# Kernel tuning notes

Hardware: AMD Instinct MI355X
Metric: run time of the kernel (lower is better)

## Reference

```python
import jax, jax.numpy as jnp
import numpy as np
from jax import lax

B = 2
H = W = 128          # resolution
N = H * W            # 16384 tokens
C = 128              # in_channels
C2 = C // 2          # 64, attention dim
G = 16               # window_size
HEADS = 8
HDIM = C2 // HEADS   # 8
EPS = 1e-5
DN = ('NCHW', 'OIHW', 'NCHW')


def setup_inputs():
    key = jax.random.key(0)
    ks = jax.random.split(key, 16)
    r = lambda i, shape, s=0.02: jax.random.normal(ks[i], shape, jnp.float32) * s
    z = lambda shape: jnp.zeros(shape, jnp.float32)
    o = lambda shape: jnp.ones(shape, jnp.float32)
    return {
        'x_C': jax.random.normal(ks[0], (B, N, C), jnp.float32),
        'x_T': jax.random.normal(ks[1], (B, N, C), jnp.float32),
        # S_conv = depthwise 3x3 + pointwise 1x1
        'conv1_dw': r(2, (C, 1, 3, 3)), 'conv1_dw_b': z((C,)),
        'conv1_pw': r(3, (C, C, 1, 1)), 'conv1_pw_b': z((C,)),
        'bn1_gamma': o((C,)), 'bn1_beta': z((C,)),
        'bn1_mean': r(4, (C,), 0.1), 'bn1_var': jnp.abs(r(5, (C,), 0.1)) + 1.0,
        'enc_W': r(6, (C, C2)), 'enc_b': z((C2,)),
        'pos': r(7, (1, N, C2)),
        'ln_gamma': o((C2,)), 'ln_beta': z((C2,)),
        'qkv_W': r(8, (C2, 3 * C2)),                      # qkv_bias=False
        'proj_W': r(9, (C2, C2)), 'proj_b': z((C2,)),
        'ffn_W1': r(10, (C2, C2)), 'ffn_b1': z((C2,)),
        'ffn_W2': r(11, (C2, C2)), 'ffn_b2': z((C2,)),
        'dec_W': r(12, (C2, C)), 'dec_b': z((C,)),
    }


def _ln(x, g, b):
    m = jnp.mean(x, -1, keepdims=True)
    v = jnp.var(x, -1, keepdims=True)
    return (x - m) * jax.lax.rsqrt(v + EPS) * g + b


def _win_part(x):  # (B,N,C2) -> (B*nW, G*G, C2)
    x = x.reshape(B, H // G, G, W // G, G, C2).transpose(0, 1, 3, 2, 4, 5)
    return x.reshape(-1, G * G, C2)


def _win_rev(x):  # (B*nW, G*G, C2) -> (B,N,C2)
    x = x.reshape(B, H // G, W // G, G, G, C2).transpose(0, 1, 3, 2, 4, 5)
    return x.reshape(B, N, C2)


def reference(x_C, x_T, conv1_dw, conv1_dw_b, conv1_pw, conv1_pw_b,
              bn1_gamma, bn1_beta, bn1_mean, bn1_var,
              enc_W, enc_b, pos, ln_gamma, ln_beta, qkv_W,
              proj_W, proj_b, ffn_W1, ffn_b1, ffn_W2, ffn_b2, dec_W, dec_b):
    cb = lambda a: a[None, :, None, None]
    # ---- CNN branch on x_C: S_conv -> BN(eval) -> ReLU, residual
    xC = x_C.reshape(B, H, W, C).transpose(0, 3, 1, 2)  # NCHW
    h = lax.conv_general_dilated(xC, conv1_dw, (1, 1), 'SAME',
                                 feature_group_count=C, dimension_numbers=DN) + cb(conv1_dw_b)
    h = lax.conv_general_dilated(h, conv1_pw, (1, 1), 'SAME',
                                 dimension_numbers=DN) + cb(conv1_pw_b)
    h = (h - cb(bn1_mean)) * cb(bn1_gamma * jax.lax.rsqrt(bn1_var + EPS)) + cb(bn1_beta)
    x1 = jax.nn.relu(h) + xC
    # ---- x_T branch: source overwrites conv/bn outputs -> x2 = relu(x_T) + x_T
    xT = x_T.reshape(B, H, W, C).transpose(0, 3, 1, 2)
    x2 = jax.nn.relu(xT) + xT
    # ---- flatten to tokens, encode + positional embedding
    x = x1.transpose(0, 2, 3, 1).reshape(B, N, C)
    y = x2.transpose(0, 2, 3, 1).reshape(B, N, C)
    x_poi = x @ enc_W + enc_b + pos
    y_poi = y @ enc_W + enc_b + pos
    # ---- window partition + LayerNorm
    wx = _ln(_win_part(x_poi), ln_gamma, ln_beta)
    wy = _ln(_win_part(y_poi), ln_gamma, ln_beta)
    # ---- dual-stream windowed attention (cross values)
    scale = HDIM ** -0.5
    def qkv(t):
        q, k, v = jnp.split(t @ qkv_W, 3, axis=-1)
        re = lambda a: a.reshape(-1, G * G, HEADS, HDIM).transpose(0, 2, 1, 3)
        return re(q), re(k), re(v)
    q, k, v = qkv(wx)
    q1, k1, v1 = qkv(wy)
    attn = jax.nn.softmax(jnp.einsum('bhid,bhjd->bhij', q * scale, k), axis=-1)
    attn1 = jax.nn.softmax(jnp.einsum('bhid,bhjd->bhij', q1 * scale, k1), axis=-1)
    ox = jnp.einsum('bhij,bhjd->bhid', attn, v1).transpose(0, 2, 1, 3).reshape(-1, G * G, C2)
    oy = jnp.einsum('bhij,bhjd->bhid', attn1, v).transpose(0, 2, 1, 3).reshape(-1, G * G, C2)
    ox = ox @ proj_W + proj_b + wx
    oy = oy @ proj_W + proj_b + wy
    # ---- window reverse + FFN (pre-LN, residual)
    x = _win_rev(ox)
    y = _win_rev(oy)
    ffn = lambda t: jax.nn.relu(_ln(t, ln_gamma, ln_beta) @ ffn_W1 + ffn_b1) @ ffn_W2 + ffn_b2
    x = x + ffn(x)
    y = y + ffn(y)
    # ---- decode back to C channels; to_3d(reshape) is identity on (B,N,C)
    return (x @ dec_W + dec_b) + (y @ dec_W + dec_b)
```

## Files before the change

### kernel.cpp

```cpp
#include <hip/hip_runtime.h>
#include <hip/hip_bf16.h>
#include <math.h>

#define EPSF 1e-5f
#define KSCL 0.51010090329771713f

#if __has_builtin(__builtin_amdgcn_exp2f)
#define EXP2(x) __builtin_amdgcn_exp2f(x)
#else
#define EXP2(x) exp2f(x)
#endif

typedef __attribute__((ext_vector_type(8))) short short8;
typedef __attribute__((ext_vector_type(16))) float f32x16;

__device__ __forceinline__ float bf2f(unsigned short u) {
    union { unsigned int i; float f; } x; x.i = ((unsigned int)u) << 16; return x.f;
}
__device__ __forceinline__ unsigned int f2bf(float f) {
    union { float f; unsigned int i; } u; u.f = f;
    unsigned int r = u.i + 0x7FFFu + ((u.i >> 16) & 1u);
    return r >> 16;
}
__device__ __forceinline__ unsigned cvtpk(float a, float b) {
    unsigned r;
    asm("v_cvt_pk_bf16_f32 %0, %1, %2" : "=v"(r) : "v"(a), "v"(b));
    return r;
}
__device__ __forceinline__ void bbuild(const unsigned pk[8], int lh,
                                       short8& B0, short8& B1) {
    unsigned xs[8];
    #pragma unroll
    for (int i = 0; i < 8; ++i) xs[i] = (unsigned)__shfl_xor((int)pk[i], 32);
    uint4 w0, w1;
    w0.x = lh ? xs[2] : pk[0]; w0.y = lh ? xs[3] : pk[1];
    w0.z = lh ? pk[2] : xs[0]; w0.w = lh ? pk[3] : xs[1];
    w1.x = lh ? xs[6] : pk[4]; w1.y = lh ? xs[7] : pk[5];
    w1.z = lh ? pk[6] : xs[4]; w1.w = lh ? pk[7] : xs[5];
    B0 = __builtin_bit_cast(short8, w0);
    B1 = __builtin_bit_cast(short8, w1);
}

__global__ __launch_bounds__(256) void k_dwconv(
    const float* __restrict__ xC, const float* __restrict__ dwW,
    const float* __restrict__ dwB, unsigned short* __restrict__ xdwb,
    const float* __restrict__ qkvW, const float* __restrict__ pw,
    const float* __restrict__ pwb, const float* __restrict__ gam,
    const float* __restrict__ bet, const float* __restrict__ mean,
    const float* __restrict__ var, const float* __restrict__ projW,
    const float* __restrict__ W1, const float* __restrict__ W2,
    const float* __restrict__ decW, const float* __restrict__ encW,
    unsigned short* __restrict__ qkvWT, unsigned short* __restrict__ weff,
    float* __restrict__ beff, unsigned short* __restrict__ projWTn,
    unsigned short* __restrict__ W1Tn, unsigned short* __restrict__ W2Tn,
    unsigned short* __restrict__ decTn, unsigned short* __restrict__ encWTn)
{
    int tid = threadIdx.x;
    int bid = blockIdx.x;
    if (bid >= 1024) {
        int pid = (bid - 1024) * 256 + tid;
        if (pid < 12288) {
            int o = pid >> 6, c = pid & 63;
            qkvWT[pid] = (unsigned short)f2bf(qkvW[c * 192 + o]);
        } else if (pid < 28672) {
            int i = pid - 12288;
            int co = i >> 7;
            float sc = gam[co] * rsqrtf(var[co] + EPSF);
            weff[i] = (unsigned short)f2bf(pw[i] * sc);
        } else if (pid < 32768) {
            int i = pid - 28672, m = i >> 6, c = i & 63;
            projWTn[i] = (unsigned short)f2bf(projW[c * 64 + m]);
        } else if (pid < 36864) {
            int i = pid - 32768, m = i >> 6, c = i & 63;
            W1Tn[i] = (unsigned short)f2bf(W1[c * 64 + m]);
        } else if (pid < 40960) {
            int i = pid - 36864, m = i >> 6, c = i & 63;
            W2Tn[i] = (unsigned short)f2bf(W2[c * 64 + m]);
        } else if (pid < 49152) {
            int i = pid - 40960, m = i >> 6, c = i & 63;
            decTn[i] = (unsigned short)f2bf(decW[c * 128 + m]);
        } else if (pid < 57344) {
            int i = pid - 49152, m = i >> 7, c = i & 127;
            encWTn[i] = (unsigned short)f2bf(encW[c * 64 + m]);
        } else if (pid < 57472) {
            int i = pid - 57344;
            float sc = gam[i] * rsqrtf(var[i] + EPSF);
            beff[i] = (pwb[i] - mean[i]) * sc + bet[i];
        }
        return;
    }
    __shared__ float s_w[128 * 9];
    __shared__ float s_bias[128];
    for (int i = tid; i < 128 * 9; i += 256) s_w[i] = dwW[i];
    if (tid < 128) s_bias[tid] = dwB[tid];
    __syncthreads();
    int idx = bid * 256 + tid;
    int c4 = (idx & 31) * 4;
    int pg = idx >> 5;
    int t0 = pg * 4;
    int b = t0 >> 14, n = t0 & 16383;
    int row = n >> 7, col0 = n & 127;
    float vb[3][6][4];
    #pragma unroll
    for (int ky = 0; ky < 3; ++ky) {
        int r = row + ky - 1;
        #pragma unroll
        for (int cx = 0; cx < 6; ++cx) {
            int cl = col0 + cx - 1;
            if ((unsigned)r < 128u && (unsigned)cl < 128u) {
                *(float4*)&vb[ky][cx][0] =
                    *(const float4*)&xC[((size_t)(b << 14) + (r << 7) + cl) * 128 + c4];
            } else {
                vb[ky][cx][0] = 0.f; vb[ky][cx][1] = 0.f; vb[ky][cx][2] = 0.f; vb[ky][cx][3] = 0.f;
            }
        }
    }
    float acc[4][4];
    #pragma unroll
    for (int p = 0; p < 4; ++p)
        #pragma unroll
        for (int j = 0; j < 4; ++j) acc[p][j] = s_bias[c4 + j];
    #pragma unroll
    for (int ky = 0; ky < 3; ++ky)
        #pragma unroll
        for (int kx = 0; kx < 3; ++kx)
            #pragma unroll
            for (int j = 0; j < 4; ++j) {
                float w = s_w[(c4 + j) * 9 + ky * 3 + kx];
                #pragma unroll
                for (int p = 0; p < 4; ++p)
                    acc[p][j] = fmaf(w, vb[ky][p + kx][j], acc[p][j]);
            }
    #pragma unroll
    for (int p = 0; p < 4; ++p) {
        uint2 o;
        o.x = f2bf(acc[p][0]) | (f2bf(acc[p][1]) << 16);
        o.y = f2bf(acc[p][2]) | (f2bf(acc[p][3]) << 16);
        *(uint2*)&xdwb[((size_t)t0 + p) * 128 + c4] = o;
    }
}

__global__ __launch_bounds__(256) void k_pw(
    const unsigned short* __restrict__ xdwb, const float* __restrict__ xC,
    const unsigned short* __restrict__ weff, const float* __restrict__ beff,
    unsigned short* __restrict__ x1b)
{
    int tid = threadIdx.x;
    int wv = tid >> 6, lane = tid & 63, l31 = lane & 31, lh = lane >> 5;
    int wr = wv >> 1, wc = wv & 1;
    int T0 = blockIdx.x * 64;
    int ta = T0 + wr * 32 + l31;
    short8 af[8];
    #pragma unroll
    for (int ks = 0; ks < 8; ++ks)
        af[ks] = *(const short8*)&xdwb[(size_t)ta * 128 + ks * 16 + lh * 8];
    #pragma unroll
    for (int nt = 0; nt < 2; ++nt) {
        int co = wc * 64 + nt * 32 + l31;
        f32x16 acc = {};
        #pragma unroll
        for (int ks = 0; ks < 8; ++ks) {
            short8 bfr = *(const short8*)&weff[(size_t)co * 128 + ks * 16 + lh * 8];
            acc = __builtin_amdgcn_mfma_f32_32x32x16_bf16(af[ks], bfr, acc, 0, 0, 0);
        }
        float be = beff[co];
        #pragma unroll
        for (int r = 0; r < 16; ++r) {
            int tt = T0 + wr * 32 + (r & 3) + 8 * (r >> 2) + 4 * lh;
            float v = fmaxf(acc[r] + be, 0.f) + xC[(size_t)tt * 128 + co];
            x1b[(size_t)tt * 128 + co] = (unsigned short)f2bf(v);
        }
    }
}

__global__ __launch_bounds__(256) void k_encqkv(
    const unsigned short* __restrict__ x1b, const float* __restrict__ xT,
    const unsigned short* __restrict__ encWTn, const float* __restrict__ encb,
    const float* __restrict__ pos, const float* __restrict__ lng,
    const float* __restrict__ lnb, const unsigned short* __restrict__ qkvWT,
    unsigned short* __restrict__ wxb, unsigned short* __restrict__ wyb,
    unsigned short* __restrict__ qk, unsigned short* __restrict__ vT)
{
    int tid = threadIdx.x;
    int wv = tid >> 6, l31 = tid & 31, lh = (tid >> 5) & 1;
    int s = blockIdx.y;
    int T0 = blockIdx.x * 128;
    int t = T0 + wv * 32 + l31;
    int n = t & 16383;
    short8 bf[8];
    if (s == 0) {
        #pragma unroll
        for (int ks = 0; ks < 8; ++ks)
            bf[ks] = *(const short8*)&x1b[(size_t)t * 128 + ks * 16 + lh * 8];
    } else {
        #pragma unroll
        for (int ks = 0; ks < 8; ++ks) {
            float4 f0 = *(const float4*)&xT[(size_t)t * 128 + ks * 16 + lh * 8];
            float4 f1 = *(const float4*)&xT[(size_t)t * 128 + ks * 16 + lh * 8 + 4];
            float r0 = f0.x > 0.f ? 2.f * f0.x : f0.x;
            float r1 = f0.y > 0.f ? 2.f * f0.y : f0.y;
            float r2 = f0.z > 0.f ? 2.f * f0.z : f0.z;
            float r3 = f0.w > 0.f ? 2.f * f0.w : f0.w;
            float r4 = f1.x > 0.f ? 2.f * f1.x : f1.x;
            float r5 = f1.y > 0.f ? 2.f * f1.y : f1.y;
            float r6 = f1.z > 0.f ? 2.f * f1.z : f1.z;
            float r7 = f1.w > 0.f ? 2.f * f1.w : f1.w;
            uint4 w;
            w.x = cvtpk(r0, r1); w.y = cvtpk(r2, r3);
            w.z = cvtpk(r4, r5); w.w = cvtpk(r6, r7);
            bf[ks] = __builtin_bit_cast(short8, w);
        }
    }
    f32x16 xm[2];
    #pragma unroll
    for (int ta = 0; ta < 2; ++ta) {
        f32x16 acc = {};
        #pragma unroll
        for (int ks = 0; ks < 8; ++ks) {
            short8 af = *(const short8*)&encWTn[(size_t)(ta * 32 + l31) * 128 + ks * 16 + lh * 8];
            acc = __builtin_amdgcn_mfma_f32_32x32x16_bf16(af, bf[ks], acc, 0, 0, 0);
        }
        #pragma unroll
        for (int g = 0; g < 4; ++g) {
            int c0 = ta * 32 + g * 8 + lh * 4;
            float4 eb = *(const float4*)&encb[c0];
            float4 pv = *(const float4*)&pos[(size_t)n * 64 + c0];
            acc[g * 4 + 0] += eb.x + pv.x;
            acc[g * 4 + 1] += eb.y + pv.y;
            acc[g * 4 + 2] += eb.z + pv.z;
            acc[g * 4 + 3] += eb.w + pv.w;
        }
        xm[ta] = acc;
    }
    float sm = 0.f, sq = 0.f;
    #pragma unroll
    for (int ta = 0; ta < 2; ++ta)
        #pragma unroll
        for (int r = 0; r < 16; ++r) { float v = xm[ta][r]; sm += v; sq += v * v; }
    sm += __shfl_xor(sm, 32); sq += __shfl_xor(sq, 32);
    float mu = sm * (1.f / 64.f);
    float rs = rsqrtf(fmaxf(sq * (1.f / 64.f) - mu * mu, 0.f) + EPSF);
    unsigned short* dstb = s ? wyb : wxb;
    unsigned pku[2][8];
    #pragma unroll
    for (int ta = 0; ta < 2; ++ta)
        #pragma unroll
        for (int g = 0; g < 4; ++g) {
            int c0 = ta * 32 + g * 8 + lh * 4;
            float4 gg = *(const float4*)&lng[c0];
            float4 bb = *(const float4*)&lnb[c0];
            float u0 = (xm[ta][g * 4 + 0] - mu) * rs * gg.x + bb.x;
            float u1 = (xm[ta][g * 4 + 1] - mu) * rs * gg.y + bb.y;
            float u2 = (xm[ta][g * 4 + 2] - mu) * rs * gg.z + bb.z;
            float u3 = (xm[ta][g * 4 + 3] - mu) * rs * gg.w + bb.w;
            pku[ta][g * 2]     = cvtpk(u0, u1);
            pku[ta][g * 2 + 1] = cvtpk(u2, u3);
            uint2 o; o.x = pku[ta][g * 2]; o.y = pku[ta][g * 2 + 1];
            *(uint2*)&dstb[(size_t)t * 64 + c0] = o;
        }
    short8 Bu[4];
    bbuild(pku[0], lh, Bu[0], Bu[1]);
    bbuild(pku[1], lh, Bu[2], Bu[3]);
    int b = T0 >> 14;
    int row = (T0 & 16383) >> 7;
    int cp = wv * 32 + l31;
    int wid = ((row >> 4) << 3) + (cp >> 4);
    int p = ((row & 15) << 4) + (cp & 15);
    size_t cb = (size_t)(s * 2 + b) * 512 + wid;
    #pragma unroll
    for (int nt = 0; nt < 6; ++nt) {
        f32x16 acc = {};
        #pragma unroll
        for (int ks = 0; ks < 4; ++ks) {
            short8 afr = *(const short8*)&qkvWT[(size_t)(nt * 32 + l31) * 64 + ks * 16 + lh * 8];
            acc = __builtin_amdgcn_mfma_f32_32x32x16_bf16(afr, Bu[ks], acc, 0, 0, 0);
        }
        if (nt < 4) {
            const float scl = nt < 2 ? 1.f : KSCL;
            const int sec = nt < 2 ? 0 : 1;
            #pragma unroll
            for (int g = 0; g < 4; ++g) {
                int head = (nt & 1) * 4 + g;
                unsigned short* rec = qk + (cb + head * 64) * 4096;
                float f0 = acc[4 * g + 0] * scl, f1 = acc[4 * g + 1] * scl;
                float f2 = acc[4 * g + 2] * scl, f3 = acc[4 * g + 3] * scl;
                unsigned u01 = cvtpk(f0, f1), u23 = cvtpk(f2, f3);
                int off = p * 16 + sec * 8 + 4 * lh;
                *(unsigned*)(rec + off) = u01;
                *(unsigned*)(rec + off + 2) = u23;
            }
        } else {
            #pragma unroll
            for (int g = 0; g < 4; ++g) {
                int head = (nt - 4) * 4 + g;
                unsigned short* vrec = vT + (cb + head * 64) * 2048;
                int d0 = 4 * lh;
                vrec[(d0 + 0) * 256 + p] = (unsigned short)f2bf(acc[4 * g + 0]);
                vrec[(d0 + 1) * 256 + p] = (unsigned short)f2bf(acc[4 * g + 1]);
                vrec[(d0 + 2) * 256 + p] = (unsigned short)f2bf(acc[4 * g + 2]);
                vrec[(d0 + 3) * 256 + p] = (unsigned short)f2bf(acc[4 * g + 3]);
            }
        }
    }
}

__global__ __launch_bounds__(256) void k_attn(
    const unsigned short* __restrict__ qk, const unsigned short* __restrict__ vT,
    unsigned short* __restrict__ obx, unsigned short* __restrict__ oby)
{
    int tid = threadIdx.x;
    int wave = tid >> 6, lane = tid & 63;
    int lh = lane >> 5, l31 = lane & 31;
    int bx = blockIdx.x;
    int s = bx >> 10;
    int r = bx & 1023;
    int head = (r >> 6) & 7, wid = r & 63, b = r >> 9;
    const unsigned short* qbase = qk + ((size_t)s * 1024 + r) * 4096;
    const unsigned short* vbase = vT + ((size_t)(s ^ 1) * 1024 + r) * 2048;

    short8 qf[2];
    #pragma unroll
    for (int qt = 0; qt < 2; ++qt) {
        uint4 v = {0u, 0u, 0u, 0u};
        if (lh == 0) v = *(const uint4*)(qbase + (size_t)(wave * 64 + qt * 32 + l31) * 16);
        qf[qt] = __builtin_bit_cast(short8, v);
    }
    f32x16 acc[2];
    #pragma unroll
    for (int qt = 0; qt < 2; ++qt) acc[qt] = (f32x16){};
    const unsigned ONES = 0x3F803F80u;

    for (int jt = 0; jt < 8; ++jt) {
        uint4 kv = {0u, 0u, 0u, 0u};
        if (lh == 0) kv = *(const uint4*)(qbase + (size_t)(jt * 32 + l31) * 16 + 8);
        short8 kf = __builtin_bit_cast(short8, kv);
        uint2 a0 = {ONES, ONES}, a1 = {ONES, ONES}, a2 = {ONES, ONES}, a3 = {ONES, ONES};
        if (l31 < 8) {
            const unsigned short* vp = vbase + l31 * 256 + jt * 32 + lh * 4;
            a0 = *(const uint2*)vp;
            a1 = *(const uint2*)(vp + 8);
            a2 = *(const uint2*)(vp + 16);
            a3 = *(const uint2*)(vp + 24);
        }
        uint4 vaw = {a0.x, a0.y, a1.x, a1.y};
        uint4 vbw = {a2.x, a2.y, a3.x, a3.y};
        short8 vf0 = __builtin_bit_cast(short8, vaw);
        short8 vf1 = __builtin_bit_cast(short8, vbw);
        #pragma unroll
        for (int qt = 0; qt < 2; ++qt) {
            f32x16 c = __builtin_amdgcn_mfma_f32_32x32x16_bf16(kf, qf[qt], (f32x16){}, 0, 0, 0);
            float p[16];
            #pragma unroll
            for (int i = 0; i < 16; ++i) p[i] = EXP2(c[i]);
            unsigned pk[8];
            #pragma unroll
            for (int i = 0; i < 8; ++i) pk[i] = cvtpk(p[2 * i], p[2 * i + 1]);
            uint4 bw0 = {pk[0], pk[1], pk[2], pk[3]};
            uint4 bw1 = {pk[4], pk[5], pk[6], pk[7]};
            short8 B0 = __builtin_bit_cast(short8, bw0);
            short8 B1 = __builtin_bit_cast(short8, bw1);
            acc[qt] = __builtin_amdgcn_mfma_f32_32x32x16_bf16(vf0, B0, acc[qt], 0, 0, 0);
            acc[qt] = __builtin_amdgcn_mfma_f32_32x32x16_bf16(vf1, B1, acc[qt], 0, 0, 0);
        }
    }
    unsigned short* dst = s ? oby : obx;
    #pragma unroll
    for (int qt = 0; qt < 2; ++qt) {
        float inv = 1.f / acc[qt][4];
        int p = wave * 64 + qt * 32 + l31;
        int orow = (wid >> 3) * 16 + (p >> 4);
        int ocol = (wid & 7) * 16 + (p & 15);
        size_t t = (size_t)b * 16384 + orow * 128 + ocol;
        uint2 o;
        o.x = cvtpk(acc[qt][0] * inv, acc[qt][1] * inv);
        o.y = cvtpk(acc[qt][2] * inv, acc[qt][3] * inv);
        *(uint2*)&dst[t * 64 + head * 8 + lh * 4] = o;
    }
}

__global__ __launch_bounds__(256) void k_fusedec(
    const unsigned short* __restrict__ obx, const unsigned short* __restrict__ oby,
    const unsigned short* __restrict__ wxb, const unsigned short* __restrict__ wyb,
    const unsigned short* __restrict__ projWTn, const float* __restrict__ projb,
    const unsigned short* __restrict__ W1Tn, const float* __restrict__ b1,
    const unsigned short* __restrict__ W2Tn, const float* __restrict__ b2,
    const unsigned short* __restrict__ decTn, const float* __restrict__ decb,
    const float* __restrict__ lng, const float* __restrict__ lnb,
    float* __restrict__ out)
{
    int tid = threadIdx.x;
    int wv = tid >> 6, l31 = tid & 31, lh = (tid >> 5) & 1;
    int t = blockIdx.x * 128 + wv * 32 + l31;
    f32x16 zacc[2];
    zacc[0] = (f32x16){}; zacc[1] = (f32x16){};
    #pragma unroll 1
    for (int s = 0; s < 2; ++s) {
        const unsigned short* osrc = s ? oby : obx;
        const unsigned short* wsrc = s ? wyb : wxb;
        short8 bo[4];
        #pragma unroll
        for (int kap = 0; kap < 4; ++kap)
            bo[kap] = *(const short8*)&osrc[(size_t)t * 64 + kap * 16 + lh * 8];
        f32x16 a1[2];
        #pragma unroll
        for (int ta = 0; ta < 2; ++ta) {
            f32x16 acc = {};
            #pragma unroll
            for (int kap = 0; kap < 4; ++kap) {
                short8 af = *(const short8*)&projWTn[(size_t)(ta * 32 + l31) * 64 + kap * 16 + lh * 8];
                acc = __builtin_amdgcn_mfma_f32_32x32x16_bf16(af, bo[kap], acc, 0, 0, 0);
            }
            #pragma unroll
            for (int g = 0; g < 4; ++g) {
                int c0 = ta * 32 + g * 8 + lh * 4;
                float4 pb = *(const float4*)&projb[c0];
                uint2 wr2 = *(const uint2*)&wsrc[(size_t)t * 64 + c0];
                acc[g * 4 + 0] += pb.x + bf2f((unsigned short)(wr2.x & 0xffffu));
                acc[g * 4 + 1] += pb.y + bf2f((unsigned short)(wr2.x >> 16));
                acc[g * 4 + 2] += pb.z + bf2f((unsigned short)(wr2.y & 0xffffu));
                acc[g * 4 + 3] += pb.w + bf2f((unsigned short)(wr2.y >> 16));
            }
            a1[ta] = acc;
        }
        float sm = 0.f, sq = 0.f;
        #pragma unroll
        for (int ta = 0; ta < 2; ++ta)
            #pragma unroll
            for (int r = 0; r < 16; ++r) { float v = a1[ta][r]; sm += v; sq += v * v; }
        sm += __shfl_xor(sm, 32); sq += __shfl_xor(sq, 32);
        float mu = sm * (1.f / 64.f);
        float rs = rsqrtf(fmaxf(sq * (1.f / 64.f) - mu * mu, 0.f) + EPSF);
        unsigned pku[2][8];
        #pragma unroll
        for (int ta = 0; ta < 2; ++ta)
            #pragma unroll
            for (int g = 0; g < 4; ++g) {
                int c0 = ta * 32 + g * 8 + lh * 4;
                float4 gg = *(const float4*)&lng[c0];
                float4 bb = *(const float4*)&lnb[c0];
                float u0 = (a1[ta][g * 4 + 0] - mu) * rs * gg.x + bb.x;
                float u1 = (a1[ta][g * 4 + 1] - mu) * rs * gg.y + bb.y;
                float u2 = (a1[ta][g * 4 + 2] - mu) * rs * gg.z + bb.z;
                float u3 = (a1[ta][g * 4 + 3] - mu) * rs * gg.w + bb.w;
                pku[ta][g * 2]     = cvtpk(u0, u1);
                pku[ta][g * 2 + 1] = cvtpk(u2, u3);
            }
        short8 Bu[4];
        bbuild(pku[0], lh, Bu[0], Bu[1]);
        bbuild(pku[1], lh, Bu[2], Bu[3]);
        unsigned pkh[2][8];
        #pragma unroll
        for (int th = 0; th < 2; ++th) {
            f32x16 acc = {};
            #pragma unroll
            for (int kap = 0; kap < 4; ++kap) {
                short8 af = *(const short8*)&W1Tn[(size_t)(th * 32 + l31) * 64 + kap * 16 + lh * 8];
                acc = __builtin_amdgcn_mfma_f32_32x32x16_bf16(af, Bu[kap], acc, 0, 0, 0);
            }
            #pragma unroll
            for (int g = 0; g < 4; ++g) {
                int c0 = th * 32 + g * 8 + lh * 4;
                float4 bb = *(const float4*)&b1[c0];
                float h0 = fmaxf(acc[g * 4 + 0] + bb.x, 0.f);
                float h1 = fmaxf(acc[g * 4 + 1] + bb.y, 0.f);
                float h2 = fmaxf(acc[g * 4 + 2] + bb.z, 0.f);
                float h3 = fmaxf(acc[g * 4 + 3] + bb.w, 0.f);
                pkh[th][g * 2]     = cvtpk(h0, h1);
                pkh[th][g * 2 + 1] = cvtpk(h2, h3);
            }
        }
        short8 Bh[4];
        bbuild(pkh[0], lh, Bh[0], Bh[1]);
        bbuild(pkh[1], lh, Bh[2], Bh[3]);
        #pragma unroll
        for (int ta = 0; ta < 2; ++ta) {
            f32x16 a3 = a1[ta];
            #pragma unroll
            for (int g = 0; g < 4; ++g) {
                int c0 = ta * 32 + g * 8 + lh * 4;
                float4 bb = *(const float4*)&b2[c0];
                a3[g * 4 + 0] += bb.x; a3[g * 4 + 1] += bb.y;
                a3[g * 4 + 2] += bb.z; a3[g * 4 + 3] += bb.w;
            }
            #pragma unroll
            for (int kap = 0; kap < 4; ++kap) {
                short8 af = *(const short8*)&W2Tn[(size_t)(ta * 32 + l31) * 64 + kap * 16 + lh * 8];
                a3 = __builtin_amdgcn_mfma_f32_32x32x16_bf16(af, Bh[kap], a3, 0, 0, 0);
            }
            zacc[ta] += a3;
        }
    }
    unsigned pkz[2][8];
    #pragma unroll
    for (int ta = 0; ta < 2; ++ta)
        #pragma unroll
        for (int g = 0; g < 4; ++g) {
            pkz[ta][g * 2]     = cvtpk(zacc[ta][g * 4 + 0], zacc[ta][g * 4 + 1]);
            pkz[ta][g * 2 + 1] = cvtpk(zacc[ta][g * 4 + 2], zacc[ta][g * 4 + 3]);
        }
    short8 Bz[4];
    bbuild(pkz[0], lh, Bz[0], Bz[1]);
    bbuild(pkz[1], lh, Bz[2], Bz[3]);
    #pragma unroll
    for (int mu4 = 0; mu4 < 4; ++mu4) {
        f32x16 a4 = {};
        #pragma unroll
        for (int g = 0; g < 4; ++g) {
            int c0 = mu4 * 32 + g * 8 + lh * 4;
            float4 db = *(const float4*)&decb[c0];
            a4[g * 4 + 0] = 2.f * db.x; a4[g * 4 + 1] = 2.f * db.y;
            a4[g * 4 + 2] = 2.f * db.z; a4[g * 4 + 3] = 2.f * db.w;
        }
        #pragma unroll
        for (int kap = 0; kap < 4; ++kap) {
            short8 af = *(const short8*)&decTn[(size_t)(mu4 * 32 + l31) * 64 + kap * 16 + lh * 8];
            a4 = __builtin_amdgcn_mfma_f32_32x32x16_bf16(af, Bz[kap], a4, 0, 0, 0);
        }
        #pragma unroll
        for (int g = 0; g < 4; ++g) {
            int c0 = mu4 * 32 + g * 8 + lh * 4;
            float4 o;
            o.x = a4[g * 4 + 0]; o.y = a4[g * 4 + 1];
            o.z = a4[g * 4 + 2]; o.w = a4[g * 4 + 3];
            *(float4*)&out[(size_t)t * 128 + c0] = o;
        }
    }
}

extern "C" void kernel_launch(void* const* d_in, const int* in_sizes, int n_in,
                              void* d_out, int out_size, void* d_ws, size_t ws_size,
                              hipStream_t stream) {
    const float* x_C   = (const float*)d_in[0];
    const float* x_T   = (const float*)d_in[1];
    const float* dwW   = (const float*)d_in[2];
    const float* dwB   = (const float*)d_in[3];
    const float* pw    = (const float*)d_in[4];
    const float* pwb   = (const float*)d_in[5];
    const float* gam   = (const float*)d_in[6];
    const float* bet   = (const float*)d_in[7];
    const float* mean  = (const float*)d_in[8];
    const float* var   = (const float*)d_in[9];
    const float* encW  = (const float*)d_in[10];
    const float* encb  = (const float*)d_in[11];
    const float* pos   = (const float*)d_in[12];
    const float* lng   = (const float*)d_in[13];
    const float* lnb   = (const float*)d_in[14];
    const float* qkvW  = (const float*)d_in[15];
    const float* projW = (const float*)d_in[16];
    const float* projb = (const float*)d_in[17];
    const float* W1    = (const float*)d_in[18];
    const float* b1    = (const float*)d_in[19];
    const float* W2    = (const float*)d_in[20];
    const float* b2    = (const float*)d_in[21];
    const float* decW  = (const float*)d_in[22];
    const float* decb  = (const float*)d_in[23];
    float* out = (float*)d_out;

    float* ws = (float*)d_ws;
    unsigned short* xdwb = (unsigned short*)ws;
    unsigned short* x1b  = (unsigned short*)(ws + 2097152);
    unsigned short* qkb  = (unsigned short*)(ws + 4194304);
    unsigned short* vTb  = (unsigned short*)(ws + 8388608);
    unsigned short* wxb  = (unsigned short*)(ws + 10485760);
    unsigned short* wyb  = (unsigned short*)(ws + 11534336);
    unsigned short* obx  = (unsigned short*)(ws + 12582912);
    unsigned short* oby  = (unsigned short*)(ws + 13631488);
    unsigned short* qkvWT   = (unsigned short*)(ws + 16777216);
    unsigned short* weff    = (unsigned short*)(ws + 16783360);
    float*          beff    = ws + 16791552;
    unsigned short* projWTn = (unsigned short*)(ws + 16791680);
    unsigned short* W1Tn    = (unsigned short*)(ws + 16793728);
    unsigned short* W2Tn    = (unsigned short*)(ws + 16795776);
    unsigned short* decTn   = (unsigned short*)(ws + 16797824);
    unsigned short* encWTn  = (unsigned short*)(ws + 16801920);

    k_dwconv<<<1249, 256, 0, stream>>>(x_C, dwW, dwB, xdwb, qkvW, pw, pwb,
                                       gam, bet, mean, var, projW, W1, W2, decW,
                                       encW, qkvWT, weff, beff, projWTn,
                                       W1Tn, W2Tn, decTn, encWTn);
    k_pw<<<512, 256, 0, stream>>>(xdwb, x_C, weff, beff, x1b);
    k_encqkv<<<dim3(256, 2), 256, 0, stream>>>(x1b, x_T, encWTn, encb, pos,
                                               lng, lnb, qkvWT, wxb, wyb, qkb, vTb);
    k_attn<<<2048, 256, 0, stream>>>(qkb, vTb, obx, oby);
    k_fusedec<<<256, 256, 0, stream>>>(obx, oby, wxb, wyb, projWTn, projb,
                                       W1Tn, b1, W2Tn, b2, decTn, decb,
                                       lng, lnb, out);
}
```

Measured before the change: 95.67 us.

## Fuse depthwise conv and pointwise BN-ReLU GEMM into one kernel via LDS

Merges the depthwise 3x3 conv and the pointwise 1x1 MFMA GEMM into a single kernel. The depthwise result for a 32-token tile is staged in XOR-swizzled shared memory instead of a global bf16 intermediate. The folded BN scale and bias are computed inline, and each block converts pw weights to bf16 from fp32, so the separate weff/beff prep disappears. This removes one launch and a global write and read of the intermediate. In exchange every block re-reads and converts the full pw weight matrix, and the GEMM tile per block shrinks.

```diff
diff --git a/kernel.cpp b/kernel.cpp
--- a/kernel.cpp
+++ b/kernel.cpp
@@ -41,17 +41,17 @@
     B1 = __builtin_bit_cast(short8, w1);
 }
 
-__global__ __launch_bounds__(256) void k_dwconv(
+__global__ __launch_bounds__(256) void k_dwpw(
     const float* __restrict__ xC, const float* __restrict__ dwW,
-    const float* __restrict__ dwB, unsigned short* __restrict__ xdwb,
-    const float* __restrict__ qkvW, const float* __restrict__ pw,
-    const float* __restrict__ pwb, const float* __restrict__ gam,
-    const float* __restrict__ bet, const float* __restrict__ mean,
-    const float* __restrict__ var, const float* __restrict__ projW,
-    const float* __restrict__ W1, const float* __restrict__ W2,
-    const float* __restrict__ decW, const float* __restrict__ encW,
-    unsigned short* __restrict__ qkvWT, unsigned short* __restrict__ weff,
-    float* __restrict__ beff, unsigned short* __restrict__ projWTn,
+    const float* __restrict__ dwB, const float* __restrict__ qkvW,
+    const float* __restrict__ pw, const float* __restrict__ pwb,
+    const float* __restrict__ gam, const float* __restrict__ bet,
+    const float* __restrict__ mean, const float* __restrict__ var,
+    const float* __restrict__ projW, const float* __restrict__ W1,
+    const float* __restrict__ W2, const float* __restrict__ decW,
+    const float* __restrict__ encW,
+    unsigned short* __restrict__ x1b,
+    unsigned short* __restrict__ qkvWT, unsigned short* __restrict__ projWTn,
     unsigned short* __restrict__ W1Tn, unsigned short* __restrict__ W2Tn,
     unsigned short* __restrict__ decTn, unsigned short* __restrict__ encWTn)
 {
@@ -62,42 +62,33 @@
         if (pid < 12288) {
             int o = pid >> 6, c = pid & 63;
             qkvWT[pid] = (unsigned short)f2bf(qkvW[c * 192 + o]);
-        } else if (pid < 28672) {
-            int i = pid - 12288;
-            int co = i >> 7;
-            float sc = gam[co] * rsqrtf(var[co] + EPSF);
-            weff[i] = (unsigned short)f2bf(pw[i] * sc);
+        } else if (pid < 16384) {
+            int i = pid - 12288, m = i >> 6, c = i & 63;
+            projWTn[i] = (unsigned short)f2bf(projW[c * 64 + m]);
+        } else if (pid < 20480) {
+            int i = pid - 16384, m = i >> 6, c = i & 63;
+            W1Tn[i] = (unsigned short)f2bf(W1[c * 64 + m]);
+        } else if (pid < 24576) {
+            int i = pid - 20480, m = i >> 6, c = i & 63;
+            W2Tn[i] = (unsigned short)f2bf(W2[c * 64 + m]);
         } else if (pid < 32768) {
-            int i = pid - 28672, m = i >> 6, c = i & 63;
-            projWTn[i] = (unsigned short)f2bf(projW[c * 64 + m]);
-        } else if (pid < 36864) {
-            int i = pid - 32768, m = i >> 6, c = i & 63;
-            W1Tn[i] = (unsigned short)f2bf(W1[c * 64 + m]);
-        } else if (pid < 40960) {
-            int i = pid - 36864, m = i >> 6, c = i & 63;
-            W2Tn[i] = (unsigned short)f2bf(W2[c * 64 + m]);
-        } else if (pid < 49152) {
-            int i = pid - 40960, m = i >> 6, c = i & 63;
+            int i = pid - 24576, m = i >> 6, c = i & 63;
             decTn[i] = (unsigned short)f2bf(decW[c * 128 + m]);
-        } else if (pid < 57344) {
-            int i = pid - 49152, m = i >> 7, c = i & 127;
+        } else {
+            int i = pid - 32768, m = i >> 7, c = i & 127;
             encWTn[i] = (unsigned short)f2bf(encW[c * 64 + m]);
-        } else if (pid < 57472) {
-            int i = pid - 57344;
-            float sc = gam[i] * rsqrtf(var[i] + EPSF);
-            beff[i] = (pwb[i] - mean[i]) * sc + bet[i];
         }
         return;
     }
     __shared__ float s_w[128 * 9];
     __shared__ float s_bias[128];
+    __shared__ unsigned short s_t[32 * 128];
     for (int i = tid; i < 128 * 9; i += 256) s_w[i] = dwW[i];
     if (tid < 128) s_bias[tid] = dwB[tid];
     __syncthreads();
-    int idx = bid * 256 + tid;
-    int c4 = (idx & 31) * 4;
-    int pg = idx >> 5;
-    int t0 = pg * 4;
+    int c4 = (tid & 31) * 4;
+    int T0 = bid * 32;
+    int t0 = T0 + (tid >> 5) * 4;
     int b = t0 >> 14, n = t0 & 16383;
     int row = n >> 7, col0 = n & 127;
     float vb[3][6][4];
@@ -133,43 +124,39 @@
             }
     #pragma unroll
     for (int p = 0; p < 4; ++p) {
+        int tok = (tid >> 5) * 4 + p;
         uint2 o;
         o.x = f2bf(acc[p][0]) | (f2bf(acc[p][1]) << 16);
         o.y = f2bf(acc[p][2]) | (f2bf(acc[p][3]) << 16);
-        *(uint2*)&xdwb[((size_t)t0 + p) * 128 + c4] = o;
-    }
-}
-
-__global__ __launch_bounds__(256) void k_pw(
-    const unsigned short* __restrict__ xdwb, const float* __restrict__ xC,
-    const unsigned short* __restrict__ weff, const float* __restrict__ beff,
-    unsigned short* __restrict__ x1b)
-{
-    int tid = threadIdx.x;
+        unsigned off = (tok << 8) + (c4 << 1);
+        off ^= ((tok & 7) << 4);
+        *(uint2*)((char*)s_t + off) = o;
+    }
+    __syncthreads();
     int wv = tid >> 6, lane = tid & 63, l31 = lane & 31, lh = lane >> 5;
-    int wr = wv >> 1, wc = wv & 1;
-    int T0 = blockIdx.x * 64;
-    int ta = T0 + wr * 32 + l31;
-    short8 af[8];
-    #pragma unroll
-    for (int ks = 0; ks < 8; ++ks)
-        af[ks] = *(const short8*)&xdwb[(size_t)ta * 128 + ks * 16 + lh * 8];
-    #pragma unroll
-    for (int nt = 0; nt < 2; ++nt) {
-        int co = wc * 64 + nt * 32 + l31;
-        f32x16 acc = {};
-        #pragma unroll
-        for (int ks = 0; ks < 8; ++ks) {
-            short8 bfr = *(const short8*)&weff[(size_t)co * 128 + ks * 16 + lh * 8];
-            acc = __builtin_amdgcn_mfma_f32_32x32x16_bf16(af[ks], bfr, acc, 0, 0, 0);
-        }
-        float be = beff[co];
-        #pragma unroll
-        for (int r = 0; r < 16; ++r) {
-            int tt = T0 + wr * 32 + (r & 3) + 8 * (r >> 2) + 4 * lh;
-            float v = fmaxf(acc[r] + be, 0.f) + xC[(size_t)tt * 128 + co];
-            x1b[(size_t)tt * 128 + co] = (unsigned short)f2bf(v);
-        }
+    int co = wv * 32 + l31;
+    float sc = gam[co] * rsqrtf(var[co] + EPSF);
+    float be = (pwb[co] - mean[co]) * sc + bet[co];
+    f32x16 acc2 = {};
+    #pragma unroll
+    for (int ks = 0; ks < 8; ++ks) {
+        const float* pwp = &pw[(size_t)co * 128 + ks * 16 + lh * 8];
+        float4 p0 = *(const float4*)pwp;
+        float4 p1 = *(const float4*)(pwp + 4);
+        uint4 w;
+        w.x = cvtpk(p0.x * sc, p0.y * sc); w.y = cvtpk(p0.z * sc, p0.w * sc);
+        w.z = cvtpk(p1.x * sc, p1.y * sc); w.w = cvtpk(p1.z * sc, p1.w * sc);
+        short8 bfr = __builtin_bit_cast(short8, w);
+        unsigned roff = (l31 << 8) + (ks << 5) + (lh << 4);
+        roff ^= ((l31 & 7) << 4);
+        short8 afr = *(const short8*)((const char*)s_t + roff);
+        acc2 = __builtin_amdgcn_mfma_f32_32x32x16_bf16(afr, bfr, acc2, 0, 0, 0);
+    }
+    #pragma unroll
+    for (int r = 0; r < 16; ++r) {
+        int tt = T0 + (r & 3) + 8 * (r >> 2) + 4 * lh;
+        float v = fmaxf(acc2[r] + be, 0.f) + xC[(size_t)tt * 128 + co];
+        x1b[(size_t)tt * 128 + co] = (unsigned short)f2bf(v);
     }
 }
 
@@ -557,7 +544,6 @@
     float* out = (float*)d_out;
 
     float* ws = (float*)d_ws;
-    unsigned short* xdwb = (unsigned short*)ws;
     unsigned short* x1b  = (unsigned short*)(ws + 2097152);
     unsigned short* qkb  = (unsigned short*)(ws + 4194304);
     unsigned short* vTb  = (unsigned short*)(ws + 8388608);
@@ -566,19 +552,16 @@
     unsigned short* obx  = (unsigned short*)(ws + 12582912);
     unsigned short* oby  = (unsigned short*)(ws + 13631488);
     unsigned short* qkvWT   = (unsigned short*)(ws + 16777216);
-    unsigned short* weff    = (unsigned short*)(ws + 16783360);
-    float*          beff    = ws + 16791552;
     unsigned short* projWTn = (unsigned short*)(ws + 16791680);
     unsigned short* W1Tn    = (unsigned short*)(ws + 16793728);
     unsigned short* W2Tn    = (unsigned short*)(ws + 16795776);
     unsigned short* decTn   = (unsigned short*)(ws + 16797824);
     unsigned short* encWTn  = (unsigned short*)(ws + 16801920);
 
-    k_dwconv<<<1249, 256, 0, stream>>>(x_C, dwW, dwB, xdwb, qkvW, pw, pwb,
-                                       gam, bet, mean, var, projW, W1, W2, decW,
-                                       encW, qkvWT, weff, beff, projWTn,
-                                       W1Tn, W2Tn, decTn, encWTn);
-    k_pw<<<512, 256, 0, stream>>>(xdwb, x_C, weff, beff, x1b);
+    k_dwpw<<<1184, 256, 0, stream>>>(x_C, dwW, dwB, qkvW, pw, pwb,
+                                     gam, bet, mean, var, projW, W1, W2, decW,
+                                     encW, x1b, qkvWT, projWTn,
+                                     W1Tn, W2Tn, decTn, encWTn);
     k_encqkv<<<dim3(256, 2), 256, 0, stream>>>(x1b, x_T, encWTn, encb, pos,
                                                lng, lnb, qkvWT, wxb, wyb, qkb, vTb);
     k_attn<<<2048, 256, 0, stream>>>(qkb, vTb, obx, oby);
```

Result: faster. 93.32 us (median of 2 runs) (-2.5%).
